# Kernel tuning notes

Hardware: AMD Instinct MI355X
Metric: run time of the kernel (lower is better)

The kernel has to match this reference:

```python
import jax, jax.numpy as jnp
import numpy as np

B, H, S, D = 8, 16, 1024, 128

def setup_inputs() -> dict:
    key = jax.random.key(0)
    kq, kk, kv = jax.random.split(key, 3)
    q = jax.random.normal(kq, (B, H, S, D), dtype=jnp.float32)
    k = jax.random.normal(kk, (B, H, S, D), dtype=jnp.float32)
    v = jax.random.normal(kv, (B, H, S, D), dtype=jnp.float32)
    return {"q": q, "k": k, "v": v}

def reference(q, k, v):
    dims = q.shape[-1]
    # scores[..., j, i] = sum_k q[..., j, k] * k_[..., i, k]; note scale is 1/dims (not 1/sqrt(dims))
    scores = jnp.einsum('bhjd,bhid->bhji', q, k) / dims
    probs = jax.nn.softmax(scores, axis=-1)
    out = jnp.einsum('bhji,bhid->bhjd', probs, v)
    return out
```

## Files before the change

kernel.cpp:

```cpp
#include <hip/hip_runtime.h>

#define S_LEN 1024
#define D_DIM 128
#define KVBLK 64
#define QROWS_BLK 128
#define BH_N 128
#define M0_LOG2 2.0f

typedef __attribute__((ext_vector_type(8))) short short8;
typedef __attribute__((ext_vector_type(4))) short short4v;
typedef __attribute__((ext_vector_type(4))) float f32x4;

__device__ __forceinline__ unsigned short f2bf(float f) {
  union { float f; unsigned u; } x; x.f = f;
  unsigned r = x.u + 0x7fffu + ((x.u >> 16) & 1u);
  return (unsigned short)(r >> 16);
}

__device__ __forceinline__ short8 pack8(float4 a, float4 b) {
  short8 f;
  f[0] = (short)f2bf(a.x); f[1] = (short)f2bf(a.y);
  f[2] = (short)f2bf(a.z); f[3] = (short)f2bf(a.w);
  f[4] = (short)f2bf(b.x); f[5] = (short)f2bf(b.y);
  f[6] = (short)f2bf(b.z); f[7] = (short)f2bf(b.w);
  return f;
}

__device__ __forceinline__ void gload_lds16(const void* g, void* l) {
  __builtin_amdgcn_global_load_lds(
      (const __attribute__((address_space(1))) unsigned int*)g,
      (__attribute__((address_space(3))) unsigned int*)l, 16, 0, 0);
}

__global__ __launch_bounds__(256) void conv_k(const float* __restrict__ in,
                                              unsigned short* __restrict__ out,
                                              int n8) {
  int i = blockIdx.x * 256 + threadIdx.x;
  int stride = gridDim.x * 256;
  for (; i < n8; i += stride) {
    float4 a = ((const float4*)in)[i * 2];
    float4 b = ((const float4*)in)[i * 2 + 1];
    ((short8*)out)[i] = pack8(a, b);
  }
}

__global__ __launch_bounds__(256) void conv_vt(const float* __restrict__ v,
                                               unsigned short* __restrict__ vt) {
  __shared__ unsigned short tile[64][72];
  int b = blockIdx.x;
  int d0 = (b & 1) * 64;
  int s0 = ((b >> 1) & 15) * 64;
  int bh = b >> 5;
  int t = threadIdx.x;
  #pragma unroll
  for (int i = 0; i < 4; ++i) {
    int s = (t >> 4) + i * 16;
    int dl = (t & 15) * 4;
    float4 x = *(const float4*)(v + ((size_t)(bh * S_LEN) + s0 + s) * D_DIM + d0 + dl);
    tile[s][dl + 0] = f2bf(x.x); tile[s][dl + 1] = f2bf(x.y);
    tile[s][dl + 2] = f2bf(x.z); tile[s][dl + 3] = f2bf(x.w);
  }
  __syncthreads();
  #pragma unroll
  for (int i = 0; i < 2; ++i) {
    int j = i * 256 + t;
    int dl = j >> 3, sc = j & 7;
    short8 w;
    #pragma unroll
    for (int q = 0; q < 8; ++q) w[q] = (short)tile[sc * 8 + q][dl];
    *(short8*)(vt + ((size_t)(bh * D_DIM) + d0 + dl) * S_LEN + s0 + sc * 8) = w;
  }
}

__global__ __launch_bounds__(512, 4) void attn_main(
    const float* __restrict__ qg, const unsigned short* __restrict__ kbf,
    const unsigned short* __restrict__ vtbf, float* __restrict__ og) {
  __shared__ unsigned short K_lds[2][KVBLK * D_DIM];
  __shared__ unsigned short VT_lds[2][D_DIM * KVBLK];
  __shared__ unsigned short P_lds[8][16 * KVBLK];

  const int tid = threadIdx.x;
  const int lane = tid & 63;
  const int wid = tid >> 6;
  const int l15 = lane & 15;
  const int lg = lane >> 4;

  const int bid = blockIdx.x;
  const int bh = (bid & 7) | ((bid >> 6) << 3);
  const int qt = (bid >> 3) & 7;

  const size_t base = (size_t)bh * (S_LEN * D_DIM);
  const int qw = qt * QROWS_BLK + wid * 16;

  short8 qf[4];
  {
    const float* qp = qg + base + (size_t)(qw + l15) * D_DIM + lg * 8;
    const float s = 0.0078125f * 1.44269504088896f;
    #pragma unroll
    for (int c = 0; c < 4; ++c) {
      float4 a = *(const float4*)(qp + c * 32);
      float4 b = *(const float4*)(qp + c * 32 + 4);
      a.x *= s; a.y *= s; a.z *= s; a.w *= s;
      b.x *= s; b.y *= s; b.z *= s; b.w *= s;
      qf[c] = pack8(a, b);
    }
  }

  float neg_m[4];
  float l_r[4];
  f32x4 o_acc[8];
  #pragma unroll
  for (int r = 0; r < 4; ++r) { neg_m[r] = -M0_LOG2; l_r[r] = 0.f; }
  #pragma unroll
  for (int dt = 0; dt < 8; ++dt) o_acc[dt] = (f32x4){0.f, 0.f, 0.f, 0.f};

  const unsigned short* kb = kbf + (size_t)bh * (S_LEN * D_DIM);
  const unsigned short* vtb = vtbf + (size_t)bh * (D_DIM * S_LEN);

  #define STAGE(buf, kv0)                                                      \
    {                                                                          \
      _Pragma("unroll")                                                        \
      for (int i = 0; i < 2; ++i) {                                            \
        int row = wid * 8 + i * 4 + (lane >> 4);                               \
        int c = lane & 15;                                                     \
        const unsigned short* src =                                            \
            kb + (size_t)((kv0) + row) * D_DIM + ((c ^ (row & 7)) * 8);        \
        gload_lds16(src, &K_lds[buf][(wid * 8 + i * 4) * D_DIM]);              \
      }                                                                        \
      _Pragma("unroll")                                                        \
      for (int i = 0; i < 2; ++i) {                                            \
        int drow = wid * 16 + i * 8 + (lane >> 3);                             \
        int c = lane & 7;                                                      \
        const unsigned short* src =                                            \
            vtb + (size_t)drow * S_LEN + (kv0) + ((c ^ (drow & 7)) * 8);       \
        gload_lds16(src, &VT_lds[buf][(wid * 16 + i * 8) * KVBLK]);            \
      }                                                                        \
    }

  STAGE(0, 0);
  __syncthreads();

  #pragma unroll 2
  for (int t = 0; t < S_LEN / KVBLK; ++t) {
    const int cur = t & 1;
    if (t + 1 < S_LEN / KVBLK) STAGE(cur ^ 1, (t + 1) * KVBLK);

    f32x4 nm = (f32x4){neg_m[0], neg_m[1], neg_m[2], neg_m[3]};
    f32x4 sacc[4];
    #pragma unroll
    for (int tc = 0; tc < 4; ++tc) sacc[tc] = nm;
    #pragma unroll
    for (int tc = 0; tc < 4; ++tc) {
      int row = tc * 16 + l15;
      #pragma unroll
      for (int ck = 0; ck < 4; ++ck) {
        int sidx = row * 128 + ((ck * 32 + lg * 8) ^ ((row & 7) << 3));
        short8 kf = *(const short8*)&K_lds[cur][sidx];
        sacc[tc] = __builtin_amdgcn_mfma_f32_16x16x32_bf16(qf[ck], kf, sacc[tc], 0, 0, 0);
      }
    }

    float lmax = sacc[0][0];
    #pragma unroll
    for (int tc = 0; tc < 4; ++tc) {
      #pragma unroll
      for (int r = 0; r < 4; ++r) lmax = fmaxf(lmax, sacc[tc][r]);
    }
    if (__any(lmax > 0.f)) {
      #pragma unroll
      for (int r = 0; r < 4; ++r) {
        float a = fmaxf(fmaxf(sacc[0][r], sacc[1][r]), fmaxf(sacc[2][r], sacc[3][r]));
        a = fmaxf(a, __shfl_xor(a, 1));
        a = fmaxf(a, __shfl_xor(a, 2));
        a = fmaxf(a, __shfl_xor(a, 4));
        a = fmaxf(a, __shfl_xor(a, 8));
        float g = fmaxf(a, 0.f);
        float alpha = exp2f(-g);
        neg_m[r] -= g;
        l_r[r] *= alpha;
        #pragma unroll
        for (int dt = 0; dt < 8; ++dt) o_acc[dt][r] *= alpha;
        #pragma unroll
        for (int tc = 0; tc < 4; ++tc) sacc[tc][r] -= g;
      }
    }

    #pragma unroll
    for (int tc = 0; tc < 4; ++tc) {
      #pragma unroll
      for (int r = 0; r < 4; ++r) {
        float p = exp2f(sacc[tc][r]);
        l_r[r] += p;
        int prow = lg * 4 + r;
        int pcol = tc * 16 + l15;
        P_lds[wid][prow * 64 + (pcol ^ (((prow >> 2) & 3) << 4))] = f2bf(p);
      }
    }

    #pragma unroll
    for (int kc = 0; kc < 2; ++kc) {
      int pidx = l15 * 64 + ((kc * 32 + lg * 8) ^ (((l15 >> 2) & 3) << 4));
      short8 pf = *(const short8*)&P_lds[wid][pidx];
      #pragma unroll
      for (int dt = 0; dt < 8; ++dt) {
        int vrow = dt * 16 + l15;
        int vidx = vrow * 64 + ((kc * 32 + lg * 8) ^ ((vrow & 7) << 3));
        short8 vf = *(const short8*)&VT_lds[cur][vidx];
        o_acc[dt] = __builtin_amdgcn_mfma_f32_16x16x32_bf16(pf, vf, o_acc[dt], 0, 0, 0);
      }
    }
    __syncthreads();
  }

  float linv[4];
  #pragma unroll
  for (int r = 0; r < 4; ++r) {
    float s = l_r[r];
    s += __shfl_xor(s, 1); s += __shfl_xor(s, 2);
    s += __shfl_xor(s, 4); s += __shfl_xor(s, 8);
    linv[r] = 1.0f / s;
  }
  #pragma unroll
  for (int r = 0; r < 4; ++r) {
    float* op = og + base + (size_t)(qw + lg * 4 + r) * D_DIM + l15;
    #pragma unroll
    for (int dt = 0; dt < 8; ++dt) op[dt * 16] = o_acc[dt][r] * linv[r];
  }
}

__global__ __launch_bounds__(256) void attn_fused(
    const float* __restrict__ qg, const float* __restrict__ kg,
    const float* __restrict__ vg, float* __restrict__ og) {
  __shared__ unsigned short K_lds[KVBLK * D_DIM];
  __shared__ unsigned short VT_lds[D_DIM * KVBLK];
  __shared__ unsigned short P_lds[4][16 * KVBLK];

  const int tid = threadIdx.x;
  const int lane = tid & 63;
  const int wid = tid >> 6;
  const int l15 = lane & 15;
  const int lg = lane >> 4;

  const int bid = blockIdx.x;
  const int bh = (bid & 7) | ((bid >> 7) << 3);
  const int qt = (bid >> 3) & 15;

  const size_t base = (size_t)bh * (S_LEN * D_DIM);
  const int qw = qt * 64 + wid * 16;

  short8 qf[4];
  {
    const float* qp = qg + base + (size_t)(qw + l15) * D_DIM + lg * 8;
    #pragma unroll
    for (int c = 0; c < 4; ++c) {
      float4 a = *(const float4*)(qp + c * 32);
      float4 b = *(const float4*)(qp + c * 32 + 4);
      const float s = 0.0078125f;
      a.x *= s; a.y *= s; a.z *= s; a.w *= s;
      b.x *= s; b.y *= s; b.z *= s; b.w *= s;
      qf[c] = pack8(a, b);
    }
  }

  float m_r[4], l_r[4];
  f32x4 o_acc[8];
  #pragma unroll
  for (int r = 0; r < 4; ++r) { m_r[r] = -INFINITY; l_r[r] = 0.f; }
  #pragma unroll
  for (int dt = 0; dt < 8; ++dt) o_acc[dt] = (f32x4){0.f, 0.f, 0.f, 0.f};

  for (int kv0 = 0; kv0 < S_LEN; kv0 += KVBLK) {
    {
      const float* kb = kg + base + (size_t)kv0 * D_DIM;
      #pragma unroll
      for (int c = tid; c < KVBLK * D_DIM / 8; c += 256) {
        int row = c >> 4, dc = c & 15;
        const float* p = kb + row * D_DIM + dc * 8;
        float4 a = *(const float4*)p;
        float4 b = *(const float4*)(p + 4);
        int sidx = row * 128 + ((dc * 8) ^ ((row & 7) << 3));
        *(short8*)&K_lds[sidx] = pack8(a, b);
      }
    }
    {
      const float* vb = vg + base + (size_t)kv0 * D_DIM;
      #pragma unroll
      for (int u = tid; u < (KVBLK / 4) * (D_DIM / 4); u += 256) {
        int ib = u & 15;
        int db = u >> 4;
        const float* p = vb + (ib * 4) * D_DIM + db * 4;
        float rr[4][4];
        #pragma unroll
        for (int c = 0; c < 4; ++c) {
          float4 t = *(const float4*)(p + c * D_DIM);
          rr[c][0] = t.x; rr[c][1] = t.y; rr[c][2] = t.z; rr[c][3] = t.w;
        }
        #pragma unroll
        for (int j = 0; j < 4; ++j) {
          short4v w;
          w[0] = (short)f2bf(rr[0][j]); w[1] = (short)f2bf(rr[1][j]);
          w[2] = (short)f2bf(rr[2][j]); w[3] = (short)f2bf(rr[3][j]);
          int row = db * 4 + j;
          int sidx = row * 64 + ((ib * 4) ^ ((row & 7) << 3));
          *(short4v*)&VT_lds[sidx] = w;
        }
      }
    }
    __syncthreads();

    f32x4 sacc[4];
    #pragma unroll
    for (int tc = 0; tc < 4; ++tc) sacc[tc] = (f32x4){0.f, 0.f, 0.f, 0.f};
    #pragma unroll
    for (int tc = 0; tc < 4; ++tc) {
      int row = tc * 16 + l15;
      #pragma unroll
      for (int ck = 0; ck < 4; ++ck) {
        int sidx = row * 128 + ((ck * 32 + lg * 8) ^ ((row & 7) << 3));
        short8 kf = *(const short8*)&K_lds[sidx];
        sacc[tc] = __builtin_amdgcn_mfma_f32_16x16x32_bf16(qf[ck], kf, sacc[tc], 0, 0, 0);
      }
    }

    float alpha[4], ps[4];
    #pragma unroll
    for (int r = 0; r < 4; ++r) {
      float a = fmaxf(fmaxf(sacc[0][r], sacc[1][r]), fmaxf(sacc[2][r], sacc[3][r]));
      a = fmaxf(a, __shfl_xor(a, 1));
      a = fmaxf(a, __shfl_xor(a, 2));
      a = fmaxf(a, __shfl_xor(a, 4));
      a = fmaxf(a, __shfl_xor(a, 8));
      float mn = fmaxf(m_r[r], a);
      alpha[r] = __expf(m_r[r] - mn);
      m_r[r] = mn;
      ps[r] = 0.f;
    }
    #pragma unroll
    for (int tc = 0; tc < 4; ++tc) {
      #pragma unroll
      for (int r = 0; r < 4; ++r) {
        float p = __expf(sacc[tc][r] - m_r[r]);
        ps[r] += p;
        int prow = lg * 4 + r;
        int pcol = tc * 16 + l15;
        P_lds[wid][prow * 64 + (pcol ^ ((prow & 7) << 3))] = f2bf(p);
      }
    }
    #pragma unroll
    for (int r = 0; r < 4; ++r) {
      float s = ps[r];
      s += __shfl_xor(s, 1); s += __shfl_xor(s, 2);
      s += __shfl_xor(s, 4); s += __shfl_xor(s, 8);
      l_r[r] = l_r[r] * alpha[r] + s;
    }
    #pragma unroll
    for (int dt = 0; dt < 8; ++dt) {
      #pragma unroll
      for (int r = 0; r < 4; ++r) o_acc[dt][r] *= alpha[r];
    }

    #pragma unroll
    for (int kc = 0; kc < 2; ++kc) {
      int pidx = l15 * 64 + ((kc * 32 + lg * 8) ^ ((l15 & 7) << 3));
      short8 pf = *(const short8*)&P_lds[wid][pidx];
      #pragma unroll
      for (int dt = 0; dt < 8; ++dt) {
        int vrow = dt * 16 + l15;
        int vidx = vrow * 64 + ((kc * 32 + lg * 8) ^ ((vrow & 7) << 3));
        short8 vf = *(const short8*)&VT_lds[vidx];
        o_acc[dt] = __builtin_amdgcn_mfma_f32_16x16x32_bf16(pf, vf, o_acc[dt], 0, 0, 0);
      }
    }
    __syncthreads();
  }

  #pragma unroll
  for (int r = 0; r < 4; ++r) {
    float inv = 1.0f / l_r[r];
    float* op = og + base + (size_t)(qw + lg * 4 + r) * D_DIM + l15;
    #pragma unroll
    for (int dt = 0; dt < 8; ++dt) op[dt * 16] = o_acc[dt][r] * inv;
  }
}

extern "C" void kernel_launch(void* const* d_in, const int* in_sizes, int n_in,
                              void* d_out, int out_size, void* d_ws, size_t ws_size,
                              hipStream_t stream) {
  const float* q = (const float*)d_in[0];
  const float* k = (const float*)d_in[1];
  const float* v = (const float*)d_in[2];
  float* o = (float*)d_out;

  const size_t n_elem = (size_t)BH_N * S_LEN * D_DIM;
  const size_t need = 2 * n_elem * sizeof(unsigned short);

  if (ws_size >= need) {
    unsigned short* kbf = (unsigned short*)d_ws;
    unsigned short* vtbf = kbf + n_elem;
    conv_k<<<dim3(2048), dim3(256), 0, stream>>>(k, kbf, (int)(n_elem / 8));
    conv_vt<<<dim3(4096), dim3(256), 0, stream>>>(v, vtbf);
    attn_main<<<dim3(1024), dim3(512), 0, stream>>>(q, kbf, vtbf, o);
  } else {
    attn_fused<<<dim3(2048), dim3(256), 0, stream>>>(q, k, v, o);
  }
}
```

Before: 155.2 us.

## Transpose QK MFMA so each lane owns one query row for softmax

Swaps the MFMA operands so the score tile comes out transposed, with each lane holding four key columns of a single query row. The row max and row sum then need only two cross-lane shuffles instead of four shuffles per row, and the running max and sum become scalars per lane. The probabilities are packed to bf16 with v_cvt_pk_bf16_f32 and written to LDS as 8-byte stores under a new swizzle, replacing scalar 2-byte stores. The rescale of the output accumulator still needs a per-row shuffle broadcast of the correction factor, which adds some work on the rescale path.

```diff
diff --git a/kernel.cpp b/kernel.cpp
--- a/kernel.cpp
+++ b/kernel.cpp
@@ -106,11 +106,9 @@
     }
   }
 
-  float neg_m[4];
-  float l_r[4];
+  float neg_m = -M0_LOG2;
+  float l_r = 0.f;
   f32x4 o_acc[8];
-  #pragma unroll
-  for (int r = 0; r < 4; ++r) { neg_m[r] = -M0_LOG2; l_r[r] = 0.f; }
   #pragma unroll
   for (int dt = 0; dt < 8; ++dt) o_acc[dt] = (f32x4){0.f, 0.f, 0.f, 0.f};
 
@@ -140,15 +138,16 @@
   STAGE(0, 0);
   __syncthreads();
 
+  char* const pwave = (char*)&P_lds[wid][0];
+
   #pragma unroll 2
   for (int t = 0; t < S_LEN / KVBLK; ++t) {
     const int cur = t & 1;
     if (t + 1 < S_LEN / KVBLK) STAGE(cur ^ 1, (t + 1) * KVBLK);
 
-    f32x4 nm = (f32x4){neg_m[0], neg_m[1], neg_m[2], neg_m[3]};
     f32x4 sacc[4];
     #pragma unroll
-    for (int tc = 0; tc < 4; ++tc) sacc[tc] = nm;
+    for (int tc = 0; tc < 4; ++tc) sacc[tc] = (f32x4){neg_m, neg_m, neg_m, neg_m};
     #pragma unroll
     for (int tc = 0; tc < 4; ++tc) {
       int row = tc * 16 + l15;
@@ -156,7 +155,7 @@
       for (int ck = 0; ck < 4; ++ck) {
         int sidx = row * 128 + ((ck * 32 + lg * 8) ^ ((row & 7) << 3));
         short8 kf = *(const short8*)&K_lds[cur][sidx];
-        sacc[tc] = __builtin_amdgcn_mfma_f32_16x16x32_bf16(qf[ck], kf, sacc[tc], 0, 0, 0);
+        sacc[tc] = __builtin_amdgcn_mfma_f32_16x16x32_bf16(kf, qf[ck], sacc[tc], 0, 0, 0);
       }
     }
 
@@ -167,40 +166,46 @@
       for (int r = 0; r < 4; ++r) lmax = fmaxf(lmax, sacc[tc][r]);
     }
     if (__any(lmax > 0.f)) {
-      #pragma unroll
-      for (int r = 0; r < 4; ++r) {
-        float a = fmaxf(fmaxf(sacc[0][r], sacc[1][r]), fmaxf(sacc[2][r], sacc[3][r]));
-        a = fmaxf(a, __shfl_xor(a, 1));
-        a = fmaxf(a, __shfl_xor(a, 2));
-        a = fmaxf(a, __shfl_xor(a, 4));
-        a = fmaxf(a, __shfl_xor(a, 8));
-        float g = fmaxf(a, 0.f);
-        float alpha = exp2f(-g);
-        neg_m[r] -= g;
-        l_r[r] *= alpha;
+      float a = lmax;
+      a = fmaxf(a, __shfl_xor(a, 16));
+      a = fmaxf(a, __shfl_xor(a, 32));
+      float delta = fmaxf(a, 0.f);
+      neg_m -= delta;
+      l_r *= exp2f(-delta);
+      float ar[4];
+      #pragma unroll
+      for (int r = 0; r < 4; ++r)
+        ar[r] = exp2f(-__shfl(delta, lg * 4 + r, 16));
+      #pragma unroll
+      for (int dt = 0; dt < 8; ++dt) {
         #pragma unroll
-        for (int dt = 0; dt < 8; ++dt) o_acc[dt][r] *= alpha;
+        for (int r = 0; r < 4; ++r) o_acc[dt][r] *= ar[r];
+      }
+      #pragma unroll
+      for (int tc = 0; tc < 4; ++tc) {
         #pragma unroll
-        for (int tc = 0; tc < 4; ++tc) sacc[tc][r] -= g;
+        for (int r = 0; r < 4; ++r) sacc[tc][r] -= delta;
       }
     }
 
     #pragma unroll
     for (int tc = 0; tc < 4; ++tc) {
-      #pragma unroll
-      for (int r = 0; r < 4; ++r) {
-        float p = exp2f(sacc[tc][r]);
-        l_r[r] += p;
-        int prow = lg * 4 + r;
-        int pcol = tc * 16 + l15;
-        P_lds[wid][prow * 64 + (pcol ^ (((prow >> 2) & 3) << 4))] = f2bf(p);
-      }
+      float p0 = exp2f(sacc[tc][0]);
+      float p1 = exp2f(sacc[tc][1]);
+      float p2 = exp2f(sacc[tc][2]);
+      float p3 = exp2f(sacc[tc][3]);
+      l_r += (p0 + p1) + (p2 + p3);
+      unsigned w0, w1;
+      asm("v_cvt_pk_bf16_f32 %0, %1, %2" : "=v"(w0) : "v"(p0), "v"(p1));
+      asm("v_cvt_pk_bf16_f32 %0, %1, %2" : "=v"(w1) : "v"(p2), "v"(p3));
+      int pb = l15 * 128 + ((tc * 32 + lg * 8) ^ ((l15 & 7) << 4));
+      *(uint2*)(pwave + pb) = make_uint2(w0, w1);
     }
 
     #pragma unroll
     for (int kc = 0; kc < 2; ++kc) {
-      int pidx = l15 * 64 + ((kc * 32 + lg * 8) ^ (((l15 >> 2) & 3) << 4));
-      short8 pf = *(const short8*)&P_lds[wid][pidx];
+      int pbr = l15 * 128 + ((kc * 64 + lg * 16) ^ ((l15 & 7) << 4));
+      short8 pf = *(const short8*)(pwave + pbr);
       #pragma unroll
       for (int dt = 0; dt < 8; ++dt) {
         int vrow = dt * 16 + l15;
@@ -212,19 +217,18 @@
     __syncthreads();
   }
 
-  float linv[4];
-  #pragma unroll
-  for (int r = 0; r < 4; ++r) {
-    float s = l_r[r];
-    s += __shfl_xor(s, 1); s += __shfl_xor(s, 2);
-    s += __shfl_xor(s, 4); s += __shfl_xor(s, 8);
-    linv[r] = 1.0f / s;
-  }
+  float lsum = l_r;
+  lsum += __shfl_xor(lsum, 16);
+  lsum += __shfl_xor(lsum, 32);
+  float linv = 1.0f / lsum;
+  float lr[4];
+  #pragma unroll
+  for (int r = 0; r < 4; ++r) lr[r] = __shfl(linv, lg * 4 + r, 16);
   #pragma unroll
   for (int r = 0; r < 4; ++r) {
     float* op = og + base + (size_t)(qw + lg * 4 + r) * D_DIM + l15;
     #pragma unroll
-    for (int dt = 0; dt < 8; ++dt) op[dt * 16] = o_acc[dt][r] * linv[r];
+    for (int dt = 0; dt < 8; ++dt) op[dt * 16] = o_acc[dt][r] * lr[r];
   }
 }
 
```

Result: faster. 136.6 us (-12.0%).
